# Kernel tuning notes

Measured on AMD Instinct MI355X. Metric: run time of the kernel, lower is better.

Reference implementation:

```python
import jax, jax.numpy as jnp
import numpy as np


def xenet_batch(x, a, e, sw, sb, aiw, aib, ajw, ajb, nw, nb, ew, eb):
    """Spektral XENetConvBatch: x (B,N,F), a (B,N,N), e (B,N,N,S)."""
    B, N, F = x.shape
    x_i = jnp.broadcast_to(x[:, :, None, :], (B, N, N, F))   # target node i per pair
    x_j = jnp.broadcast_to(x[:, None, :, :], (B, N, N, F))   # source node j per pair
    e_t = jnp.transpose(e, (0, 2, 1, 3))                      # reversed edge features
    stack = jnp.concatenate([x_i, x_j, e, e_t], axis=-1)      # (B,N,N,2F+2S)
    stack = jax.nn.relu(stack @ sw + sb)                      # stack MLP, (B,N,N,32)
    stack = stack * a[..., None]                              # mask/weight by adjacency
    att_i = jax.nn.sigmoid(stack @ aiw + aib)                 # incoming gate
    att_j = jax.nn.sigmoid(stack @ ajw + ajb)                 # outgoing gate
    agg_i = jnp.sum(att_i * stack, axis=2)                    # aggregate over sources j -> (B,N,32)
    agg_j = jnp.sum(att_j * stack, axis=1)                    # aggregate over targets i -> (B,N,32)
    x_out = jnp.concatenate([x, agg_i, agg_j], axis=-1) @ nw + nb  # node model (linear)
    e_out = stack @ ew + eb                                   # edge model (linear)
    return x_out, e_out


def setup_inputs() -> dict:
    key = jax.random.key(0)
    ks = jax.random.split(key, 16)
    B, N, F, S, C, L = 1, 400, 240, 1, 32, 1440
    SIN = 2 * F + 2 * S   # 482
    NIN = F + 2 * C       # 304
    s = 0.05
    inp = {
        "x": jax.random.normal(ks[0], (B, N, F), jnp.float32),
        "a": jax.random.uniform(ks[1], (B, N, N), jnp.float32),
        "e": jax.random.normal(ks[2], (B, N, N, S), jnp.float32),
        "c1_sw": jax.random.normal(ks[3], (SIN, C), jnp.float32) * s,
        "c1_sb": jnp.zeros((C,), jnp.float32),
        "c1_aiw": jax.random.normal(ks[4], (C, 1), jnp.float32) * s,
        "c1_aib": jnp.zeros((1,), jnp.float32),
        "c1_ajw": jax.random.normal(ks[5], (C, 1), jnp.float32) * s,
        "c1_ajb": jnp.zeros((1,), jnp.float32),
        "c1_nw": jax.random.normal(ks[6], (NIN, F), jnp.float32) * s,
        "c1_nb": jnp.zeros((F,), jnp.float32),
        "c1_ew": jax.random.normal(ks[7], (C, S), jnp.float32) * s,
        "c1_eb": jnp.zeros((S,), jnp.float32),
        "c2_sw": jax.random.normal(ks[8], (SIN, C), jnp.float32) * s,
        "c2_sb": jnp.zeros((C,), jnp.float32),
        "c2_aiw": jax.random.normal(ks[9], (C, 1), jnp.float32) * s,
        "c2_aib": jnp.zeros((1,), jnp.float32),
        "c2_ajw": jax.random.normal(ks[10], (C, 1), jnp.float32) * s,
        "c2_ajb": jnp.zeros((1,), jnp.float32),
        "c2_nw": jax.random.normal(ks[11], (NIN, F), jnp.float32) * s,
        "c2_nb": jnp.zeros((F,), jnp.float32),
        "c2_ew": jax.random.normal(ks[12], (C, S), jnp.float32) * s,
        "c2_eb": jnp.zeros((S,), jnp.float32),
        "dw": jax.random.normal(ks[13], (F, L), jnp.float32) * s,
        "db": jnp.zeros((L,), jnp.float32),
    }
    return inp


def reference(x, a, e,
              c1_sw, c1_sb, c1_aiw, c1_aib, c1_ajw, c1_ajb, c1_nw, c1_nb, c1_ew, c1_eb,
              c2_sw, c2_sb, c2_aiw, c2_aib, c2_ajw, c2_ajb, c2_nw, c2_nb, c2_ew, c2_eb,
              dw, db):
    x, e = xenet_batch(x, a, e, c1_sw, c1_sb, c1_aiw, c1_aib, c1_ajw, c1_ajb,
                       c1_nw, c1_nb, c1_ew, c1_eb)
    x, e = xenet_batch(x, a, e, c2_sw, c2_sb, c2_aiw, c2_aib, c2_ajw, c2_ajb,
                       c2_nw, c2_nb, c2_ew, c2_eb)
    return x @ dw + db  # (B, N, n_labels)
```

## Files before the change

### kernel.cpp

```cpp
#include <hip/hip_runtime.h>

#define NN 400
#define FF 240
#define CC 32
#define NIN 304
#define LL 1440

__global__ __launch_bounds__(256) void pq_kernel(
    const float* __restrict__ x, const float* __restrict__ sw,
    const float* __restrict__ sb, float* __restrict__ P, float* __restrict__ Q) {
    const int i   = blockIdx.x;
    const int t   = threadIdx.x;
    const int c   = t & 31;
    const int isQ = (t >> 5) & 1;
    const int g   = t >> 6;
    const float* wb = sw + (isQ ? FF * CC : 0) + c;
    float acc = (!isQ && g == 0) ? sb[c] : 0.0f;
    const float* xr = x + i * FF;
    const int f0 = g * 60;
    #pragma unroll 4
    for (int f = f0; f < f0 + 60; ++f) acc += xr[f] * wb[f * CC];
    __shared__ float red[4][64];
    red[g][t & 63] = acc;
    __syncthreads();
    if (t < 64) {
        const float s = red[0][t] + red[1][t] + red[2][t] + red[3][t];
        if (t >= 32) Q[i * CC + (t & 31)] = s;
        else         P[i * CC + t] = s;
    }
}

template<bool WRITE_E, bool DO_PQ>
__global__ __launch_bounds__(1024) void rcf_node(
    const float* __restrict__ P, const float* __restrict__ Q,
    const float* __restrict__ e, const float* __restrict__ a,
    const float* __restrict__ sw_tail,
    const float* __restrict__ aiw, const float* __restrict__ aib,
    const float* __restrict__ ajw, const float* __restrict__ ajb,
    const float* __restrict__ ew, const float* __restrict__ eb,
    float* __restrict__ e_out,
    const float* __restrict__ xin, const float* __restrict__ nw,
    const float* __restrict__ nb,
    const float* __restrict__ sw2, const float* __restrict__ sb2,
    float* __restrict__ xout, float* __restrict__ Pout, float* __restrict__ Qout) {
    const int bid  = blockIdx.x;
    const int base = (bid & 7) * 50 + (bid >> 3) * 2;
    const int t  = threadIdx.x;
    const int pg = t >> 3, l = t & 7, c0 = l * 4;

    __shared__ float red[4 * 128 * 36];
    __shared__ float part[1024];
    __shared__ float vA[304], vB[304], xsA[240], xsB[240];
    __shared__ float eout_lds[2 * NN];
    float* redn = red;
    float* red2 = red;

    if (t < FF) {
        vA[t] = xin[base * FF + t];
        vB[t] = xin[(base + 1) * FF + t];
    }

    float2 er2[4], ak2[4];
    int kk[4];
    #pragma unroll
    for (int it = 0; it < 4; ++it) {
        const int off = it * 128 + pg;
        kk[it] = (off < NN) ? off : 0;
        er2[it] = *(const float2*)(e + kk[it] * NN + base);
        ak2[it] = *(const float2*)(a + kk[it] * NN + base);
    }

    float w1v[4], w2v[4], wiv[4], wjv[4], wev[4];
    *(float4*)w1v = *(const float4*)(sw_tail + c0);
    *(float4*)w2v = *(const float4*)(sw_tail + CC + c0);
    *(float4*)wiv = *(const float4*)(aiw + c0);
    *(float4*)wjv = *(const float4*)(ajw + c0);
    if (WRITE_E) *(float4*)wev = *(const float4*)(ew + c0);
    const float bi = aib[0], bj = ajb[0];
    const float be = WRITE_E ? eb[0] : 0.0f;

    #pragma unroll
    for (int rp = 0; rp < 2; ++rp) {
        const int b = base + rp;

        float Pb[4], Qb[4];
        *(float4*)Pb = *(const float4*)(P + b * CC + c0);
        *(float4*)Qb = *(const float4*)(Q + b * CC + c0);

        float acc_i[4] = {0, 0, 0, 0}, acc_j[4] = {0, 0, 0, 0};
        #pragma unroll
        for (int it = 0; it < 4; ++it) {
            const int off = it * 128 + pg;
            const bool valid = off < NN;
            const int k = kk[it];
            float Qk[4], Pk[4];
            *(float4*)Qk = *(const float4*)(Q + k * CC + c0);
            *(float4*)Pk = *(const float4*)(P + k * CC + c0);
            const float e_f  = e[b * NN + k];
            const float a_bk = a[b * NN + k];
            const float e_r  = rp ? er2[it].y : er2[it].x;
            const float a_kb = rp ? ak2[it].y : ak2[it].x;
            float sr[4], sc[4];
            #pragma unroll
            for (int q = 0; q < 4; ++q) {
                sr[q] = fmaxf(Pb[q] + Qk[q] + e_f * w1v[q] + e_r * w2v[q], 0.0f) * a_bk;
                sc[q] = fmaxf(Pk[q] + Qb[q] + e_r * w1v[q] + e_f * w2v[q], 0.0f) * a_kb;
            }
            float d_i = sr[0] * wiv[0] + sr[1] * wiv[1] + sr[2] * wiv[2] + sr[3] * wiv[3];
            float d_j = sc[0] * wjv[0] + sc[1] * wjv[1] + sc[2] * wjv[2] + sc[3] * wjv[3];
            float d_e = WRITE_E ? (sr[0] * wev[0] + sr[1] * wev[1] + sr[2] * wev[2] + sr[3] * wev[3]) : 0.0f;
            #pragma unroll
            for (int m = 1; m < 8; m <<= 1) {
                d_i += __shfl_xor(d_i, m);
                d_j += __shfl_xor(d_j, m);
                if (WRITE_E) d_e += __shfl_xor(d_e, m);
            }
            const float gi = valid ? __fdividef(1.0f, 1.0f + __expf(-(d_i + bi))) : 0.0f;
            const float gj = valid ? __fdividef(1.0f, 1.0f + __expf(-(d_j + bj))) : 0.0f;
            #pragma unroll
            for (int q = 0; q < 4; ++q) {
                acc_i[q] += gi * sr[q];
                acc_j[q] += gj * sc[q];
            }
            if (WRITE_E && l == 0 && valid) eout_lds[rp * NN + k] = d_e + be;
        }
        #pragma unroll
        for (int q = 0; q < 4; ++q) {
            red[((rp * 2 + 0) * 128 + pg) * 36 + c0 + q] = acc_i[q];
            red[((rp * 2 + 1) * 128 + pg) * 36 + c0 + q] = acc_j[q];
        }
    }
    __syncthreads();

    if (WRITE_E && t < 2 * NN) e_out[base * NN + t] = eout_lds[t];

    {
        const int c = t & 31, sg = (t >> 5) & 7, set = t >> 8;
        float s = 0.0f;
        #pragma unroll
        for (int g2 = sg * 16; g2 < sg * 16 + 16; ++g2)
            s += red[(set * 128 + g2) * 36 + c];
        part[t] = s;
    }
    __syncthreads();

    if (t < 128) {
        const int set = t >> 5, c = t & 31;
        float s = 0.0f;
        #pragma unroll
        for (int sg = 0; sg < 8; ++sg) s += part[set * 256 + sg * 32 + c];
        float* vdst = (set < 2) ? vA : vB;
        vdst[FF + (set & 1) * CC + c] = s;
    }
    __syncthreads();

    {
        const int fg = t % 60, h = t / 60;
        if (t < 960) {
            const int f0 = fg * 4;
            float4 aA = make_float4(0.f, 0.f, 0.f, 0.f);
            float4 aB = make_float4(0.f, 0.f, 0.f, 0.f);
            const int k0 = h * 19;
            #pragma unroll
            for (int k = k0; k < k0 + 19; ++k) {
                const float4 w = *(const float4*)(nw + k * FF + f0);
                const float va = vA[k], vb = vB[k];
                aA.x += va * w.x; aA.y += va * w.y; aA.z += va * w.z; aA.w += va * w.w;
                aB.x += vb * w.x; aB.y += vb * w.y; aB.z += vb * w.z; aB.w += vb * w.w;
            }
            *(float4*)(redn + h * 240 + f0)        = aA;
            *(float4*)(redn + 3840 + h * 240 + f0) = aB;
        }
    }
    __syncthreads();
    if (t < FF) {
        float rA = nb[t], rB = nb[t];
        #pragma unroll
        for (int h = 0; h < 16; ++h) {
            rA += redn[h * 240 + t];
            rB += redn[3840 + h * 240 + t];
        }
        xout[base * FF + t]       = rA;
        xout[(base + 1) * FF + t] = rB;
        xsA[t] = rA;
        xsB[t] = rB;
    }
    if (DO_PQ) {
        __syncthreads();
        const int c = t & 31, isQ = (t >> 5) & 1, g = t >> 6;
        const float* wb = sw2 + (isQ ? FF * CC : 0) + c;
        const float bias = (!isQ && g == 0) ? sb2[c] : 0.0f;
        float accA = bias, accB = bias;
        const int f0 = g * 15;
        #pragma unroll
        for (int f = f0; f < f0 + 15; ++f) {
            const float w = wb[f * CC];
            accA += xsA[f] * w;
            accB += xsB[f] * w;
        }
        red2[g * 64 + (t & 63)]        = accA;
        red2[1024 + g * 64 + (t & 63)] = accB;
        __syncthreads();
        if (t < 128) {
            const int row = t >> 6, slot = t & 63;
            float s = 0.0f;
            #pragma unroll
            for (int g2 = 0; g2 < 16; ++g2) s += red2[row * 1024 + g2 * 64 + slot];
            const int bb = base + row;
            if (slot >= 32) Qout[bb * CC + (slot & 31)] = s;
            else            Pout[bb * CC + slot] = s;
        }
    }
}

__global__ __launch_bounds__(1024) void dense_kernel(
    const float* __restrict__ x, const float* __restrict__ dw,
    const float* __restrict__ db, float* __restrict__ out) {
    const int i0 = blockIdx.x * 8;
    const int t  = threadIdx.x;
    const int l  = t & 255;
    const int fs = t >> 8;
    const int gl = blockIdx.y * 256 + l;
    __shared__ float xs[8 * FF];
    __shared__ float red[32 * 256];
    for (int idx = t; idx < 8 * FF; idx += 1024) {
        const int r = idx / FF, f = idx - r * FF;
        xs[r * FF + f] = x[(i0 + r) * FF + f];
    }
    __syncthreads();
    float acc[8] = {0, 0, 0, 0, 0, 0, 0, 0};
    if (gl < LL) {
        const int f0 = fs * 60;
        #pragma unroll 4
        for (int f = f0; f < f0 + 60; ++f) {
            const float w = dw[f * LL + gl];
            #pragma unroll
            for (int r = 0; r < 8; ++r) acc[r] += xs[r * FF + f] * w;
        }
    }
    #pragma unroll
    for (int r = 0; r < 8; ++r) red[(fs * 8 + r) * 256 + l] = acc[r];
    __syncthreads();
    if (gl < LL) {
        const int r2 = t >> 8;
        const float d = db[gl];
        #pragma unroll
        for (int rr = r2; rr < 8; rr += 4) {
            const float s = red[(0 + rr) * 256 + l] + red[(8 + rr) * 256 + l]
                          + red[(16 + rr) * 256 + l] + red[(24 + rr) * 256 + l];
            out[(i0 + rr) * LL + gl] = d + s;
        }
    }
}

extern "C" void kernel_launch(void* const* d_in, const int* in_sizes, int n_in,
                              void* d_out, int out_size, void* d_ws, size_t ws_size,
                              hipStream_t stream) {
    const float* x  = (const float*)d_in[0];
    const float* a  = (const float*)d_in[1];
    const float* e0 = (const float*)d_in[2];

    const float* c1_sw  = (const float*)d_in[3];
    const float* c1_sb  = (const float*)d_in[4];
    const float* c1_aiw = (const float*)d_in[5];
    const float* c1_aib = (const float*)d_in[6];
    const float* c1_ajw = (const float*)d_in[7];
    const float* c1_ajb = (const float*)d_in[8];
    const float* c1_nw  = (const float*)d_in[9];
    const float* c1_nb  = (const float*)d_in[10];
    const float* c1_ew  = (const float*)d_in[11];
    const float* c1_eb  = (const float*)d_in[12];

    const float* c2_sw  = (const float*)d_in[13];
    const float* c2_sb  = (const float*)d_in[14];
    const float* c2_aiw = (const float*)d_in[15];
    const float* c2_aib = (const float*)d_in[16];
    const float* c2_ajw = (const float*)d_in[17];
    const float* c2_ajb = (const float*)d_in[18];
    const float* c2_nw  = (const float*)d_in[19];
    const float* c2_nb  = (const float*)d_in[20];
    const float* dw = (const float*)d_in[23];
    const float* db = (const float*)d_in[24];

    float* ws = (float*)d_ws;
    float* P1 = ws;
    float* Q1 = ws + 12800;
    float* P2 = ws + 25600;
    float* Q2 = ws + 38400;
    float* x1 = ws + 51200;
    float* x2 = ws + 147200;
    float* e1 = ws + 243200;

    float* out = (float*)d_out;

    pq_kernel<<<NN, 256, 0, stream>>>(x, c1_sw, c1_sb, P1, Q1);

    rcf_node<true, true><<<NN / 2, 1024, 0, stream>>>(
        P1, Q1, e0, a, c1_sw + 480 * CC,
        c1_aiw, c1_aib, c1_ajw, c1_ajb, c1_ew, c1_eb, e1,
        x, c1_nw, c1_nb, c2_sw, c2_sb, x1, P2, Q2);

    rcf_node<false, false><<<NN / 2, 1024, 0, stream>>>(
        P2, Q2, e1, a, c2_sw + 480 * CC,
        c2_aiw, c2_aib, c2_ajw, c2_ajb, nullptr, nullptr, nullptr,
        x1, c2_nw, c2_nb, nullptr, nullptr, x2, nullptr, nullptr);

    dense_kernel<<<dim3(NN / 8, 6), 1024, 0, stream>>>(x2, dw, db, out);
}
```

Before: 50.05 us.

## Fuse all four stages into one persistent kernel with hierarchical grid barrier

Replaces the four separate launches (PQ projection, two XENet layers, dense head) with a single 250-block persistent kernel. The stages are separated by a two-level atomic grid barrier whose counters are zeroed by a memset before the launch. The goal is to remove per-launch overhead and the tail gaps between kernels. The costs are spin-wait synchronisation, an extra memset, and a reliance on all 250 blocks of 1024 threads being resident at once. The PQ and dense stages are also re-tiled to fit the new block count.

```diff
diff --git a/kernel.cpp b/kernel.cpp
--- a/kernel.cpp
+++ b/kernel.cpp
@@ -5,53 +5,65 @@
 #define CC 32
 #define NIN 304
 #define LL 1440
-
-__global__ __launch_bounds__(256) void pq_kernel(
-    const float* __restrict__ x, const float* __restrict__ sw,
-    const float* __restrict__ sb, float* __restrict__ P, float* __restrict__ Q) {
-    const int i   = blockIdx.x;
-    const int t   = threadIdx.x;
-    const int c   = t & 31;
-    const int isQ = (t >> 5) & 1;
-    const int g   = t >> 6;
-    const float* wb = sw + (isQ ? FF * CC : 0) + c;
-    float acc = (!isQ && g == 0) ? sb[c] : 0.0f;
-    const float* xr = x + i * FF;
-    const int f0 = g * 60;
-    #pragma unroll 4
-    for (int f = f0; f < f0 + 60; ++f) acc += xr[f] * wb[f * CC];
-    __shared__ float red[4][64];
-    red[g][t & 63] = acc;
-    __syncthreads();
-    if (t < 64) {
-        const float s = red[0][t] + red[1][t] + red[2][t] + red[3][t];
-        if (t >= 32) Q[i * CC + (t & 31)] = s;
-        else         P[i * CC + t] = s;
-    }
+#define NB 250
+#define NGROUPS 16
+
+struct Params {
+    const float *x, *a, *e0;
+    const float *c1_sw, *c1_sb, *c1_aiw, *c1_aib, *c1_ajw, *c1_ajb;
+    const float *c1_nw, *c1_nb, *c1_ew, *c1_eb;
+    const float *c2_sw, *c2_sb, *c2_aiw, *c2_aib, *c2_ajw, *c2_ajb;
+    const float *c2_nw, *c2_nb;
+    const float *dw, *db;
+    float *out;
+    float *P1, *Q1, *P2, *Q2, *x1, *x2, *e1;
+    unsigned *bar;
+};
+
+__device__ __forceinline__ void gbar(unsigned* bar, int phase) {
+    __syncthreads();
+    if (threadIdx.x == 0) {
+        __threadfence();
+        unsigned* gcnt = bar;
+        unsigned* mcnt = bar + 256;
+        unsigned* grel = bar + 272;
+        const int g   = blockIdx.x >> 4;
+        const int gsz = min(16, NB - (g << 4));
+        const unsigned o = atomicAdd(&gcnt[g * 16], 1u);
+        if (o + 1u == (unsigned)(phase * gsz)) {
+            const unsigned m = atomicAdd(mcnt, 1u);
+            if (m + 1u == (unsigned)(phase * NGROUPS)) {
+                #pragma unroll
+                for (int g2 = 0; g2 < NGROUPS; ++g2) atomicAdd(&grel[g2 * 16], 1u);
+            }
+        }
+        while (atomicAdd(&grel[g * 16], 0u) < (unsigned)phase)
+            __builtin_amdgcn_s_sleep(8);
+        __threadfence();
+    }
+    __syncthreads();
 }
 
 template<bool WRITE_E, bool DO_PQ>
-__global__ __launch_bounds__(1024) void rcf_node(
-    const float* __restrict__ P, const float* __restrict__ Q,
-    const float* __restrict__ e, const float* __restrict__ a,
-    const float* __restrict__ sw_tail,
-    const float* __restrict__ aiw, const float* __restrict__ aib,
-    const float* __restrict__ ajw, const float* __restrict__ ajb,
-    const float* __restrict__ ew, const float* __restrict__ eb,
-    float* __restrict__ e_out,
-    const float* __restrict__ xin, const float* __restrict__ nw,
-    const float* __restrict__ nb,
-    const float* __restrict__ sw2, const float* __restrict__ sb2,
-    float* __restrict__ xout, float* __restrict__ Pout, float* __restrict__ Qout) {
-    const int bid  = blockIdx.x;
-    const int base = (bid & 7) * 50 + (bid >> 3) * 2;
+__device__ void rcf_body(const Params& p, int job, float* smem,
+                         const float* P, const float* Q, const float* e,
+                         const float* sw_tail, const float* aiw, const float* aib,
+                         const float* ajw, const float* ajb,
+                         const float* ew, const float* eb, float* e_out,
+                         const float* xin, const float* nw, const float* nb,
+                         const float* sw2, const float* sb2,
+                         float* xout, float* Pout, float* Qout) {
+    const int base = (job & 7) * 50 + (job >> 3) * 2;
     const int t  = threadIdx.x;
     const int pg = t >> 3, l = t & 7, c0 = l * 4;
 
-    __shared__ float red[4 * 128 * 36];
-    __shared__ float part[1024];
-    __shared__ float vA[304], vB[304], xsA[240], xsB[240];
-    __shared__ float eout_lds[2 * NN];
+    float* red  = smem;
+    float* part = smem + 18432;
+    float* vA   = smem + 19456;
+    float* vB   = smem + 19760;
+    float* xsA  = smem + 20064;
+    float* xsB  = smem + 20304;
+    float* eout_lds = smem + 20544;
     float* redn = red;
     float* red2 = red;
 
@@ -67,7 +79,7 @@
         const int off = it * 128 + pg;
         kk[it] = (off < NN) ? off : 0;
         er2[it] = *(const float2*)(e + kk[it] * NN + base);
-        ak2[it] = *(const float2*)(a + kk[it] * NN + base);
+        ak2[it] = *(const float2*)(p.a + kk[it] * NN + base);
     }
 
     float w1v[4], w2v[4], wiv[4], wjv[4], wev[4];
@@ -82,11 +94,9 @@
     #pragma unroll
     for (int rp = 0; rp < 2; ++rp) {
         const int b = base + rp;
-
         float Pb[4], Qb[4];
         *(float4*)Pb = *(const float4*)(P + b * CC + c0);
         *(float4*)Qb = *(const float4*)(Q + b * CC + c0);
-
         float acc_i[4] = {0, 0, 0, 0}, acc_j[4] = {0, 0, 0, 0};
         #pragma unroll
         for (int it = 0; it < 4; ++it) {
@@ -97,7 +107,7 @@
             *(float4*)Qk = *(const float4*)(Q + k * CC + c0);
             *(float4*)Pk = *(const float4*)(P + k * CC + c0);
             const float e_f  = e[b * NN + k];
-            const float a_bk = a[b * NN + k];
+            const float a_bk = p.a[b * NN + k];
             const float e_r  = rp ? er2[it].y : er2[it].x;
             const float a_kb = rp ? ak2[it].y : ak2[it].x;
             float sr[4], sc[4];
@@ -143,7 +153,6 @@
         part[t] = s;
     }
     __syncthreads();
-
     if (t < 128) {
         const int set = t >> 5, c = t & 31;
         float s = 0.0f;
@@ -213,42 +222,80 @@
     }
 }
 
-__global__ __launch_bounds__(1024) void dense_kernel(
-    const float* __restrict__ x, const float* __restrict__ dw,
-    const float* __restrict__ db, float* __restrict__ out) {
-    const int i0 = blockIdx.x * 8;
-    const int t  = threadIdx.x;
-    const int l  = t & 255;
-    const int fs = t >> 8;
-    const int gl = blockIdx.y * 256 + l;
-    __shared__ float xs[8 * FF];
-    __shared__ float red[32 * 256];
-    for (int idx = t; idx < 8 * FF; idx += 1024) {
-        const int r = idx / FF, f = idx - r * FF;
-        xs[r * FF + f] = x[(i0 + r) * FF + f];
-    }
-    __syncthreads();
-    float acc[8] = {0, 0, 0, 0, 0, 0, 0, 0};
-    if (gl < LL) {
-        const int f0 = fs * 60;
+__global__ __launch_bounds__(1024) void xenet_mono2(Params p) {
+    __shared__ float smem[21344];
+    const int bid = blockIdx.x;
+    const int t   = threadIdx.x;
+
+    if (bid < 100) {
+        const int i0 = bid * 4;
+        const int r = t >> 8, tt = t & 255;
+        const int c = tt & 31, isQ = (tt >> 5) & 1, g = tt >> 6;
+        const float* wb = p.c1_sw + (isQ ? FF * CC : 0) + c;
+        float acc = (!isQ && g == 0) ? p.c1_sb[c] : 0.0f;
+        const float* xr = p.x + (i0 + r) * FF;
+        const int f0 = g * 60;
         #pragma unroll 4
-        for (int f = f0; f < f0 + 60; ++f) {
-            const float w = dw[f * LL + gl];
-            #pragma unroll
-            for (int r = 0; r < 8; ++r) acc[r] += xs[r * FF + f] * w;
-        }
-    }
-    #pragma unroll
-    for (int r = 0; r < 8; ++r) red[(fs * 8 + r) * 256 + l] = acc[r];
-    __syncthreads();
-    if (gl < LL) {
-        const int r2 = t >> 8;
-        const float d = db[gl];
-        #pragma unroll
-        for (int rr = r2; rr < 8; rr += 4) {
-            const float s = red[(0 + rr) * 256 + l] + red[(8 + rr) * 256 + l]
-                          + red[(16 + rr) * 256 + l] + red[(24 + rr) * 256 + l];
-            out[(i0 + rr) * LL + gl] = d + s;
+        for (int f = f0; f < f0 + 60; ++f) acc += xr[f] * wb[f * CC];
+        smem[r * 256 + g * 64 + (tt & 63)] = acc;
+        __syncthreads();
+        if (tt < 64) {
+            float s = smem[r * 256 + tt] + smem[r * 256 + 64 + tt]
+                    + smem[r * 256 + 128 + tt] + smem[r * 256 + 192 + tt];
+            const int i = i0 + r;
+            if (tt >= 32) p.Q1[i * CC + (tt & 31)] = s;
+            else          p.P1[i * CC + tt] = s;
+        }
+    }
+    gbar(p.bar, 1);
+
+    if (bid < 200)
+        rcf_body<true, true>(p, bid, smem, p.P1, p.Q1, p.e0,
+            p.c1_sw + 480 * CC, p.c1_aiw, p.c1_aib, p.c1_ajw, p.c1_ajb,
+            p.c1_ew, p.c1_eb, p.e1,
+            p.x, p.c1_nw, p.c1_nb, p.c2_sw, p.c2_sb, p.x1, p.P2, p.Q2);
+    gbar(p.bar, 2);
+
+    if (bid < 200)
+        rcf_body<false, false>(p, bid, smem, p.P2, p.Q2, p.e1,
+            p.c2_sw + 480 * CC, p.c2_aiw, p.c2_aib, p.c2_ajw, p.c2_ajb,
+            nullptr, nullptr, nullptr,
+            p.x1, p.c2_nw, p.c2_nb, nullptr, nullptr, p.x2, nullptr, nullptr);
+    gbar(p.bar, 3);
+
+    {
+        const int ig = bid / 5, lb = bid % 5;
+        const int i0 = ig * 8;
+        float* xs   = smem;
+        float* dred = smem + 1920;
+        for (int idx = t; idx < 8 * FF; idx += 1024) {
+            xs[idx] = p.x2[i0 * FF + idx];
+        }
+        __syncthreads();
+        const int fs = t / 288, li = t % 288;
+        float acc[8] = {0, 0, 0, 0, 0, 0, 0, 0};
+        if (fs < 3) {
+            const int f0 = fs * 80;
+            const int gl = lb * 288 + li;
+            #pragma unroll 4
+            for (int f = f0; f < f0 + 80; ++f) {
+                const float w = p.dw[f * LL + gl];
+                #pragma unroll
+                for (int r = 0; r < 8; ++r) acc[r] += xs[r * FF + f] * w;
+            }
+            #pragma unroll
+            for (int r = 0; r < 8; ++r) dred[(fs * 8 + r) * 288 + li] = acc[r];
+        }
+        __syncthreads();
+        if (t < 288) {
+            const int gl = lb * 288 + t;
+            const float d = p.db[gl];
+            #pragma unroll
+            for (int r = 0; r < 8; ++r) {
+                const float s = dred[r * 288 + t] + dred[(8 + r) * 288 + t]
+                              + dred[(16 + r) * 288 + t];
+                p.out[(i0 + r) * LL + gl] = d + s;
+            }
         }
     }
 }
@@ -256,54 +303,43 @@
 extern "C" void kernel_launch(void* const* d_in, const int* in_sizes, int n_in,
                               void* d_out, int out_size, void* d_ws, size_t ws_size,
                               hipStream_t stream) {
-    const float* x  = (const float*)d_in[0];
-    const float* a  = (const float*)d_in[1];
-    const float* e0 = (const float*)d_in[2];
-
-    const float* c1_sw  = (const float*)d_in[3];
-    const float* c1_sb  = (const float*)d_in[4];
-    const float* c1_aiw = (const float*)d_in[5];
-    const float* c1_aib = (const float*)d_in[6];
-    const float* c1_ajw = (const float*)d_in[7];
-    const float* c1_ajb = (const float*)d_in[8];
-    const float* c1_nw  = (const float*)d_in[9];
-    const float* c1_nb  = (const float*)d_in[10];
-    const float* c1_ew  = (const float*)d_in[11];
-    const float* c1_eb  = (const float*)d_in[12];
-
-    const float* c2_sw  = (const float*)d_in[13];
-    const float* c2_sb  = (const float*)d_in[14];
-    const float* c2_aiw = (const float*)d_in[15];
-    const float* c2_aib = (const float*)d_in[16];
-    const float* c2_ajw = (const float*)d_in[17];
-    const float* c2_ajb = (const float*)d_in[18];
-    const float* c2_nw  = (const float*)d_in[19];
-    const float* c2_nb  = (const float*)d_in[20];
-    const float* dw = (const float*)d_in[23];
-    const float* db = (const float*)d_in[24];
+    Params p;
+    p.x  = (const float*)d_in[0];
+    p.a  = (const float*)d_in[1];
+    p.e0 = (const float*)d_in[2];
+    p.c1_sw  = (const float*)d_in[3];
+    p.c1_sb  = (const float*)d_in[4];
+    p.c1_aiw = (const float*)d_in[5];
+    p.c1_aib = (const float*)d_in[6];
+    p.c1_ajw = (const float*)d_in[7];
+    p.c1_ajb = (const float*)d_in[8];
+    p.c1_nw  = (const float*)d_in[9];
+    p.c1_nb  = (const float*)d_in[10];
+    p.c1_ew  = (const float*)d_in[11];
+    p.c1_eb  = (const float*)d_in[12];
+    p.c2_sw  = (const float*)d_in[13];
+    p.c2_sb  = (const float*)d_in[14];
+    p.c2_aiw = (const float*)d_in[15];
+    p.c2_aib = (const float*)d_in[16];
+    p.c2_ajw = (const float*)d_in[17];
+    p.c2_ajb = (const float*)d_in[18];
+    p.c2_nw  = (const float*)d_in[19];
+    p.c2_nb  = (const float*)d_in[20];
+    p.dw = (const float*)d_in[23];
+    p.db = (const float*)d_in[24];
+    p.out = (float*)d_out;
 
     float* ws = (float*)d_ws;
-    float* P1 = ws;
-    float* Q1 = ws + 12800;
-    float* P2 = ws + 25600;
-    float* Q2 = ws + 38400;
-    float* x1 = ws + 51200;
-    float* x2 = ws + 147200;
-    float* e1 = ws + 243200;
-
-    float* out = (float*)d_out;
-
-    pq_kernel<<<NN, 256, 0, stream>>>(x, c1_sw, c1_sb, P1, Q1);
-
-    rcf_node<true, true><<<NN / 2, 1024, 0, stream>>>(
-        P1, Q1, e0, a, c1_sw + 480 * CC,
-        c1_aiw, c1_aib, c1_ajw, c1_ajb, c1_ew, c1_eb, e1,
-        x, c1_nw, c1_nb, c2_sw, c2_sb, x1, P2, Q2);
-
-    rcf_node<false, false><<<NN / 2, 1024, 0, stream>>>(
-        P2, Q2, e1, a, c2_sw + 480 * CC,
-        c2_aiw, c2_aib, c2_ajw, c2_ajb, nullptr, nullptr, nullptr,
-        x1, c2_nw, c2_nb, nullptr, nullptr, x2, nullptr, nullptr);
-
-    dense_kernel<<<dim3(NN / 8, 6), 1024, 0, stream>>>(x2, dw, db, out);
+    p.P1 = ws;
+    p.Q1 = ws + 12800;
+    p.P2 = ws + 25600;
+    p.Q2 = ws + 38400;
+    p.x1 = ws + 51200;
+    p.x2 = ws + 147200;
+    p.e1 = ws + 243200;
+    p.bar = (unsigned*)(ws + 450000);
+
+    hipMemsetAsync((void*)p.bar, 0, 544 * sizeof(unsigned), stream);
+
+    xenet_mono2<<<NB, 1024, 0, stream>>>(p);
 }
```

Result: slower. 91.31 us (+82.4%).

## Shrink LDS and registers in rcf_node via wavefront shuffle reduction

Applied to the files above, without the earlier changes.

Replaces the two-stage LDS reduction of per-thread accumulators with an in-wavefront shuffle reduction across the 8 pair-groups, so only one lane group per wave writes partial sums. This shrinks the shared buffer from about 18K floats to 7680 and removes one sync and reduction pass. It also stops preloading the transposed e/a values into registers, loading them inside the loop instead, and raises the occupancy hint via launch_bounds(1024, 8). In exchange it adds shuffle instructions and re-reads e/a for the second row pass.

```diff
diff --git a/kernel.cpp b/kernel.cpp
--- a/kernel.cpp
+++ b/kernel.cpp
@@ -31,7 +31,7 @@
 }
 
 template<bool WRITE_E, bool DO_PQ>
-__global__ __launch_bounds__(1024) void rcf_node(
+__global__ __launch_bounds__(1024, 8) void rcf_node(
     const float* __restrict__ P, const float* __restrict__ Q,
     const float* __restrict__ e, const float* __restrict__ a,
     const float* __restrict__ sw_tail,
@@ -47,27 +47,18 @@
     const int base = (bid & 7) * 50 + (bid >> 3) * 2;
     const int t  = threadIdx.x;
     const int pg = t >> 3, l = t & 7, c0 = l * 4;
-
-    __shared__ float red[4 * 128 * 36];
-    __shared__ float part[1024];
+    const int w  = t >> 6;
+
+    __shared__ float big[7680];
     __shared__ float vA[304], vB[304], xsA[240], xsB[240];
     __shared__ float eout_lds[2 * NN];
-    float* redn = red;
-    float* red2 = red;
+    float* red  = big;
+    float* redn = big;
+    float* red2 = big;
 
     if (t < FF) {
         vA[t] = xin[base * FF + t];
         vB[t] = xin[(base + 1) * FF + t];
-    }
-
-    float2 er2[4], ak2[4];
-    int kk[4];
-    #pragma unroll
-    for (int it = 0; it < 4; ++it) {
-        const int off = it * 128 + pg;
-        kk[it] = (off < NN) ? off : 0;
-        er2[it] = *(const float2*)(e + kk[it] * NN + base);
-        ak2[it] = *(const float2*)(a + kk[it] * NN + base);
     }
 
     float w1v[4], w2v[4], wiv[4], wjv[4], wev[4];
@@ -92,14 +83,16 @@
         for (int it = 0; it < 4; ++it) {
             const int off = it * 128 + pg;
             const bool valid = off < NN;
-            const int k = kk[it];
+            const int k = valid ? off : 0;
             float Qk[4], Pk[4];
             *(float4*)Qk = *(const float4*)(Q + k * CC + c0);
             *(float4*)Pk = *(const float4*)(P + k * CC + c0);
+            const float2 er = *(const float2*)(e + k * NN + base);
+            const float2 ak = *(const float2*)(a + k * NN + base);
             const float e_f  = e[b * NN + k];
             const float a_bk = a[b * NN + k];
-            const float e_r  = rp ? er2[it].y : er2[it].x;
-            const float a_kb = rp ? ak2[it].y : ak2[it].x;
+            const float e_r  = rp ? er.y : er.x;
+            const float a_kb = rp ? ak.y : ak.x;
             float sr[4], sc[4];
             #pragma unroll
             for (int q = 0; q < 4; ++q) {
@@ -126,29 +119,29 @@
         }
         #pragma unroll
         for (int q = 0; q < 4; ++q) {
-            red[((rp * 2 + 0) * 128 + pg) * 36 + c0 + q] = acc_i[q];
-            red[((rp * 2 + 1) * 128 + pg) * 36 + c0 + q] = acc_j[q];
+            #pragma unroll
+            for (int m = 8; m < 64; m <<= 1) {
+                acc_i[q] += __shfl_xor(acc_i[q], m);
+                acc_j[q] += __shfl_xor(acc_j[q], m);
+            }
+        }
+        if ((t & 63) < 8) {
+            #pragma unroll
+            for (int q = 0; q < 4; ++q) {
+                red[((rp * 2 + 0) * 16 + w) * 36 + c0 + q] = acc_i[q];
+                red[((rp * 2 + 1) * 16 + w) * 36 + c0 + q] = acc_j[q];
+            }
         }
     }
     __syncthreads();
 
     if (WRITE_E && t < 2 * NN) e_out[base * NN + t] = eout_lds[t];
-
-    {
-        const int c = t & 31, sg = (t >> 5) & 7, set = t >> 8;
-        float s = 0.0f;
-        #pragma unroll
-        for (int g2 = sg * 16; g2 < sg * 16 + 16; ++g2)
-            s += red[(set * 128 + g2) * 36 + c];
-        part[t] = s;
-    }
-    __syncthreads();
 
     if (t < 128) {
         const int set = t >> 5, c = t & 31;
         float s = 0.0f;
         #pragma unroll
-        for (int sg = 0; sg < 8; ++sg) s += part[set * 256 + sg * 32 + c];
+        for (int w2 = 0; w2 < 16; ++w2) s += red[(set * 16 + w2) * 36 + c];
         float* vdst = (set < 2) ? vA : vB;
         vdst[FF + (set & 1) * CC + c] = s;
     }
@@ -163,10 +156,10 @@
             const int k0 = h * 19;
             #pragma unroll
             for (int k = k0; k < k0 + 19; ++k) {
-                const float4 w = *(const float4*)(nw + k * FF + f0);
+                const float4 wv = *(const float4*)(nw + k * FF + f0);
                 const float va = vA[k], vb = vB[k];
-                aA.x += va * w.x; aA.y += va * w.y; aA.z += va * w.z; aA.w += va * w.w;
-                aB.x += vb * w.x; aB.y += vb * w.y; aB.z += vb * w.z; aB.w += vb * w.w;
+                aA.x += va * wv.x; aA.y += va * wv.y; aA.z += va * wv.z; aA.w += va * wv.w;
+                aB.x += vb * wv.x; aB.y += vb * wv.y; aB.z += vb * wv.z; aB.w += vb * wv.w;
             }
             *(float4*)(redn + h * 240 + f0)        = aA;
             *(float4*)(redn + 3840 + h * 240 + f0) = aB;
@@ -194,9 +187,9 @@
         const int f0 = g * 15;
         #pragma unroll
         for (int f = f0; f < f0 + 15; ++f) {
-            const float w = wb[f * CC];
-            accA += xsA[f] * w;
-            accB += xsB[f] * w;
+            const float wv = wb[f * CC];
+            accA += xsA[f] * wv;
+            accB += xsB[f] * wv;
         }
         red2[g * 64 + (t & 63)]        = accA;
         red2[1024 + g * 64 + (t & 63)] = accB;
```

Result: slower. 106.6 us (+113.0%).
